# Kernel tuning notes

Hardware: AMD Instinct MI355X
Metric: run time of the kernel (lower is better)

The kernel has to match this reference:

```python
import jax, jax.numpy as jnp
import numpy as np

TOP_K = 32
OBS_RADIUS = 1.0
N = 4096
IN_DIM = 4


def setup_inputs() -> dict:
    key = jax.random.key(0)
    ks = jax.random.split(key, 10)
    s = 0.05
    return {
        "states": jax.random.normal(ks[0], (N, 4), jnp.float32),
        "goals": jax.random.normal(ks[1], (N, 2), jnp.float32),
        "W1": jax.random.normal(ks[2], (64, IN_DIM + 1), jnp.float32) * s,
        "b1": jnp.zeros((64,), jnp.float32),
        "W2": jax.random.normal(ks[3], (128, 64), jnp.float32) * s,
        "b2": jnp.zeros((128,), jnp.float32),
        "Wd1": jax.random.normal(ks[4], (64, 132), jnp.float32) * s,
        "bd1": jnp.zeros((64,), jnp.float32),
        "Wd2": jax.random.normal(ks[5], (128, 64), jnp.float32) * s,
        "bd2": jnp.zeros((128,), jnp.float32),
        "Wd3": jax.random.normal(ks[6], (64, 128), jnp.float32) * s,
        "bd3": jnp.zeros((64,), jnp.float32),
        "Wd4": jax.random.normal(ks[7], (4, 64), jnp.float32) * s,
        "bd4": jnp.zeros((4,), jnp.float32),
    }


def reference(states, goals, W1, b1, W2, b2, Wd1, bd1, Wd2, bd2, Wd3, bd3, Wd4, bd4):
    n = states.shape[0]
    dt = states.dtype
    # pairwise relative states + one-hot self indicator -> [N, N, 5]
    x = states[:, None, :] - states[None, :, :]
    x = jnp.concatenate([x, jnp.eye(n, dtype=dt)[:, :, None]], axis=2)
    # remove_distant_agents: keep TOP_K nearest neighbors by planar distance
    d = jnp.sqrt(jnp.sum(x[:, :, :2] ** 2, axis=2) + 1e-4)  # [N, N]
    _, idx = jax.lax.top_k(-d, TOP_K)                        # [N, K]
    xk = jnp.take_along_axis(x, idx[:, :, None], axis=1)     # [N, K, 5]
    # observation-radius mask (torch reshape [N,K,1]->[N,1,K] == transpose here)
    dist = jnp.linalg.norm(xk[:, :, :2], axis=2)             # [N, K]
    mask = (dist < OBS_RADIUS).astype(dt).reshape(n, 1, TOP_K)
    # NOTE: original uses a raw reshape [N,K,5]->[N,5,K] (not a transpose); match it
    h = xk.reshape(n, IN_DIM + 1, TOP_K)
    # pointwise (kernel-1) conv stack 5 -> 64 -> 128
    h = jax.nn.relu(jnp.einsum('oc,ncp->nop', W1, h) + b1[None, :, None])
    h = jax.nn.relu(jnp.einsum('oc,ncp->nop', W2, h) + b2[None, :, None])
    # original does torch.max(...)[1]: ARGMAX indices, promoted to float by cat
    x_local = jnp.argmax(h * mask, axis=2).astype(dt)        # [N, 128]
    rel = states[:, :2] - goals
    feat = jnp.concatenate([x_local, rel, states[:, 2:]], axis=1)  # [N, 132]
    z = jax.nn.relu(feat @ Wd1.T + bd1)
    z = jax.nn.relu(z @ Wd2.T + bd2)
    z = jax.nn.relu(z @ Wd3.T + bd3)
    z = z @ Wd4.T + bd4
    k = 2.0 * jax.nn.sigmoid(z) + 0.2                        # [N, 4] gains
    state = jnp.concatenate([rel, states[:, 2:]], axis=1)    # [N, 4]
    a_x = -(k[:, 0] * state[:, 0] + k[:, 1] * state[:, 2])
    a_y = -(k[:, 2] * state[:, 1] + k[:, 3] * state[:, 3])
    return jnp.stack([a_x, a_y], axis=1)                     # [N, 2]
```

## Files before the change

kernel.cpp:

```cpp
#include <hip/hip_runtime.h>
#include <math.h>

#define NAGENT 4096
#define TOPK 32
#define FAGB 8
#define CANDCAP 2048

__global__ __launch_bounds__(256) void topk_kernel(
    const float* __restrict__ states, int* __restrict__ idx_out)
{
    const int i = blockIdx.x;
    const int t = threadIdx.x;
    const int lane = t & 63;
    __shared__ unsigned int hist[1024];
    __shared__ unsigned int wsum[4];
    __shared__ unsigned long long cand[CANDCAP];
    __shared__ int ccount;
    __shared__ unsigned int cutB;

    #pragma unroll
    for (int u = 0; u < 4; ++u) hist[t + u * 256] = 0u;
    if (t == 0) ccount = 0;

    const float4 si = ((const float4*)states)[i];
    __syncthreads();

    unsigned int mybits[16];
    #pragma unroll
    for (int u = 0; u < 16; ++u) {
        int j = t + u * 256;
        float4 sj = ((const float4*)states)[j];
        float dx = __fsub_rn(si.x, sj.x);
        float dy = __fsub_rn(si.y, sj.y);
        float s  = __fadd_rn(__fadd_rn(__fmul_rn(dx, dx), __fmul_rn(dy, dy)), 1e-4f);
        float dv = sqrtf(s);
        mybits[u] = __float_as_uint(dv);
        unsigned int bin = (unsigned int)(dv * 256.0f);
        if (bin > 1023u) bin = 1023u;
        atomicAdd(&hist[bin], 1u);
    }
    __syncthreads();

    unsigned int h0 = hist[t * 4 + 0], h1 = hist[t * 4 + 1];
    unsigned int h2 = hist[t * 4 + 2], h3 = hist[t * 4 + 3];
    unsigned int v = h0 + h1 + h2 + h3;
    unsigned int inc = v;
    #pragma unroll
    for (int off = 1; off < 64; off <<= 1) {
        unsigned int u = __shfl_up(inc, off, 64);
        if (lane >= off) inc += u;
    }
    if (lane == 63) wsum[t >> 6] = inc;
    __syncthreads();
    unsigned int woff = 0;
    for (int w = 0; w < (t >> 6); ++w) woff += wsum[w];
    unsigned int incl = inc + woff;
    unsigned int exc  = incl - v;
    if (exc < TOPK && incl >= TOPK) {
        unsigned int cum = exc;
        unsigned int hh[4] = {h0, h1, h2, h3};
        int b = t * 4 + 3;
        #pragma unroll
        for (int q = 0; q < 4; ++q) {
            cum += hh[q];
            if (cum >= TOPK) { b = t * 4 + q; break; }
        }
        cutB = (unsigned int)b;
    }
    __syncthreads();

    const unsigned int B = cutB;
    #pragma unroll
    for (int u = 0; u < 16; ++u) {
        float dv = __uint_as_float(mybits[u]);
        unsigned int bin = (unsigned int)(dv * 256.0f);
        if (bin > 1023u) bin = 1023u;
        if (bin <= B) {
            int pos = atomicAdd(&ccount, 1);
            if (pos < CANDCAP)
                cand[pos] = ((unsigned long long)mybits[u] << 32)
                          | (unsigned int)(t + u * 256);
        }
    }
    __syncthreads();

    const int C = (ccount < CANDCAP) ? ccount : CANDCAP;
    for (int q = t; q < C; q += 256) {
        unsigned long long key = cand[q];
        int rank = 0;
        for (int r = 0; r < C; ++r) rank += (cand[r] < key) ? 1 : 0;
        if (rank < TOPK) idx_out[i * TOPK + rank] = (int)(key & 0xffffffffu);
    }
}

__global__ __launch_bounds__(256) void fused_kernel(
    const float* __restrict__ states, const float* __restrict__ goals,
    const float* __restrict__ W1,  const float* __restrict__ b1,
    const float* __restrict__ W2,  const float* __restrict__ b2,
    const float* __restrict__ Wd1, const float* __restrict__ bd1,
    const float* __restrict__ Wd2, const float* __restrict__ bd2,
    const float* __restrict__ Wd3, const float* __restrict__ bd3,
    const float* __restrict__ Wd4, const float* __restrict__ bd4,
    const int* __restrict__ idx_in, float* __restrict__ out)
{
    const int t = threadIdx.x;
    const int a = t >> 6;
    const int l = t & 63;
    const int base = blockIdx.x * FAGB;

    __shared__ __attribute__((aligned(16))) float w2a[64 * 68];
    __shared__ __attribute__((aligned(16))) float w2b[64 * 68];
    __shared__ __attribute__((aligned(16))) float w1s[320];
    __shared__ __attribute__((aligned(16))) float b1s[64];
    __shared__ __attribute__((aligned(16))) float b2s[128];
    __shared__ __attribute__((aligned(16))) float flat[4][160];
    __shared__ __attribute__((aligned(16))) float maskv[4][32];
    __shared__ __attribute__((aligned(16))) float featb[FAGB][132];
    __shared__ __attribute__((aligned(16))) float h1[4][2048];
    float* z1s = &h1[0][0];
    float* z2s = z1s + 512;
    float* z3s = z2s + 1024;
    float* kvs = z3s + 512;

    #pragma unroll
    for (int u = 0; u < 32; ++u) {
        int e = t + u * 256;
        int o = e >> 6, c = e & 63;
        float v = W2[e];
        int dst = c * 68 + ((o >> 3) << 2) + (o & 3);
        if (o & 4) w2b[dst] = v; else w2a[dst] = v;
    }
    for (int e = t; e < 320; e += 256) w1s[e] = W1[e];
    if (t < 64)  b1s[t] = b1[t];
    if (t < 128) b2s[t] = b2[t];
    __syncthreads();

    #pragma unroll
    for (int round = 0; round < 2; ++round) {
        const int g = round * 4 + a;
        const int i = base + g;

        if (l < 32) {
            int j = idx_in[i * TOPK + l];
            float4 sj  = ((const float4*)states)[j];
            float4 siv = ((const float4*)states)[i];
            float d0 = siv.x - sj.x;
            float d1 = siv.y - sj.y;
            float d2 = siv.z - sj.z;
            float d3 = siv.w - sj.w;
            flat[a][l * 5 + 0] = d0;
            flat[a][l * 5 + 1] = d1;
            flat[a][l * 5 + 2] = d2;
            flat[a][l * 5 + 3] = d3;
            flat[a][l * 5 + 4] = (j == i) ? 1.0f : 0.0f;
            float dist = sqrtf(__fadd_rn(__fmul_rn(d0, d0), __fmul_rn(d1, d1)));
            maskv[a][l] = (dist < 1.0f) ? 1.0f : 0.0f;
        } else if (l < 36) {
            int f = l - 32;
            float4 siv = ((const float4*)states)[i];
            float2 gi  = ((const float2*)goals)[i];
            float v = (f == 0) ? (siv.x - gi.x)
                    : (f == 1) ? (siv.y - gi.y)
                    : (f == 2) ? siv.z : siv.w;
            featb[g][128 + f] = v;
        }

        #pragma unroll
        for (int u = 0; u < 32; ++u) {
            int e = u * 64 + l;
            int p = e & 31, o1 = e >> 5;
            float acc = b1s[o1];
            #pragma unroll
            for (int f = 0; f < 5; ++f)
                acc += w1s[o1 * 5 + f] * flat[a][f * 32 + p];
            h1[a][o1 * 32 + p] = fmaxf(acc, 0.0f);
        }

        const int ow = l & 15;
        const int pt = l >> 4;
        float acc[8][8];
        #pragma unroll
        for (int k = 0; k < 8; ++k)
            #pragma unroll
            for (int q = 0; q < 8; ++q) acc[k][q] = 0.0f;

        for (int c4 = 0; c4 < 16; ++c4) {
            float4 wAv[4], wBv[4], hAv[4], hBv[4];
            #pragma unroll
            for (int cc = 0; cc < 4; ++cc) {
                int c = c4 * 4 + cc;
                wAv[cc] = *(const float4*)&w2a[c * 68 + ow * 4];
                wBv[cc] = *(const float4*)&w2b[c * 68 + ow * 4];
                hAv[cc] = *(const float4*)&h1[a][c * 32 + pt * 8];
                hBv[cc] = *(const float4*)&h1[a][c * 32 + pt * 8 + 4];
            }
            #pragma unroll
            for (int cc = 0; cc < 4; ++cc) {
                float wv[8] = {wAv[cc].x, wAv[cc].y, wAv[cc].z, wAv[cc].w,
                               wBv[cc].x, wBv[cc].y, wBv[cc].z, wBv[cc].w};
                float hv[8] = {hAv[cc].x, hAv[cc].y, hAv[cc].z, hAv[cc].w,
                               hBv[cc].x, hBv[cc].y, hBv[cc].z, hBv[cc].w};
                #pragma unroll
                for (int k = 0; k < 8; ++k)
                    #pragma unroll
                    for (int q = 0; q < 8; ++q)
                        acc[k][q] += wv[k] * hv[q];
            }
        }

        float4 mA = *(const float4*)&maskv[a][pt * 8];
        float4 mB = *(const float4*)&maskv[a][pt * 8 + 4];
        float mv[8] = {mA.x, mA.y, mA.z, mA.w, mB.x, mB.y, mB.z, mB.w};
        #pragma unroll
        for (int k = 0; k < 8; ++k) {
            float bb = b2s[ow * 8 + k];
            unsigned long long best = 0ull;
            #pragma unroll
            for (int q = 0; q < 8; ++q) {
                float val = fmaxf(acc[k][q] + bb, 0.0f) * mv[q];
                unsigned long long key =
                    ((unsigned long long)__float_as_uint(val) << 32)
                    | (unsigned int)(31 - (pt * 8 + q));
                if (key > best) best = key;
            }
            unsigned long long o1 = __shfl_xor(best, 16, 64); if (o1 > best) best = o1;
            unsigned long long o2 = __shfl_xor(best, 32, 64); if (o2 > best) best = o2;
            if (pt == 0) {
                int pbest = 31 - (int)(best & 63ull);
                featb[g][ow * 8 + k] = (float)pbest;
            }
        }
    }
    __syncthreads();

    const int g0 = 2 * a, g1 = 2 * a + 1;

    {
        float bb = bd1[l];
        float a0 = bb, a1 = bb;
        for (int k = 0; k < 33; ++k) {
            float4 wv = *(const float4*)&Wd1[l * 132 + 4 * k];
            float4 f0 = *(const float4*)&featb[g0][4 * k];
            float4 f1 = *(const float4*)&featb[g1][4 * k];
            a0 += wv.x * f0.x; a0 += wv.y * f0.y; a0 += wv.z * f0.z; a0 += wv.w * f0.w;
            a1 += wv.x * f1.x; a1 += wv.y * f1.y; a1 += wv.z * f1.z; a1 += wv.w * f1.w;
        }
        z1s[g0 * 64 + l] = fmaxf(a0, 0.0f);
        z1s[g1 * 64 + l] = fmaxf(a1, 0.0f);
    }

    {
        float accA0 = bd2[l], accA1 = bd2[l];
        float accB0 = bd2[l + 64], accB1 = bd2[l + 64];
        for (int k = 0; k < 16; ++k) {
            float4 wa = *(const float4*)&Wd2[l * 64 + 4 * k];
            float4 wb = *(const float4*)&Wd2[(l + 64) * 64 + 4 * k];
            float4 f0 = *(const float4*)&z1s[g0 * 64 + 4 * k];
            float4 f1 = *(const float4*)&z1s[g1 * 64 + 4 * k];
            accA0 += wa.x * f0.x; accA0 += wa.y * f0.y;
            accA0 += wa.z * f0.z; accA0 += wa.w * f0.w;
            accB0 += wb.x * f0.x; accB0 += wb.y * f0.y;
            accB0 += wb.z * f0.z; accB0 += wb.w * f0.w;
            accA1 += wa.x * f1.x; accA1 += wa.y * f1.y;
            accA1 += wa.z * f1.z; accA1 += wa.w * f1.w;
            accB1 += wb.x * f1.x; accB1 += wb.y * f1.y;
            accB1 += wb.z * f1.z; accB1 += wb.w * f1.w;
        }
        z2s[g0 * 128 + l]      = fmaxf(accA0, 0.0f);
        z2s[g0 * 128 + l + 64] = fmaxf(accB0, 0.0f);
        z2s[g1 * 128 + l]      = fmaxf(accA1, 0.0f);
        z2s[g1 * 128 + l + 64] = fmaxf(accB1, 0.0f);
    }

    {
        float bb = bd3[l];
        float a0 = bb, a1 = bb;
        for (int k = 0; k < 32; ++k) {
            float4 wv = *(const float4*)&Wd3[l * 128 + 4 * k];
            float4 f0 = *(const float4*)&z2s[g0 * 128 + 4 * k];
            float4 f1 = *(const float4*)&z2s[g1 * 128 + 4 * k];
            a0 += wv.x * f0.x; a0 += wv.y * f0.y; a0 += wv.z * f0.z; a0 += wv.w * f0.w;
            a1 += wv.x * f1.x; a1 += wv.y * f1.y; a1 += wv.z * f1.z; a1 += wv.w * f1.w;
        }
        z3s[g0 * 64 + l] = fmaxf(a0, 0.0f);
        z3s[g1 * 64 + l] = fmaxf(a1, 0.0f);
    }

    if (l < 8) {
        int gg = (l >> 2) ? g1 : g0;
        int o = l & 3;
        float acc = bd4[o];
        for (int c = 0; c < 64; ++c) acc += Wd4[o * 64 + c] * z3s[gg * 64 + c];
        kvs[gg * 4 + o] = 2.0f / (1.0f + expf(-acc)) + 0.2f;
    }
    if (l < 4) {
        int gg = (l >> 1) ? g1 : g0;
        int axis = l & 1;
        float ka = kvs[gg * 4 + 2 * axis + 0];
        float kb = kvs[gg * 4 + 2 * axis + 1];
        float rel = featb[gg][128 + axis];
        float vel = featb[gg][130 + axis];
        out[(base + gg) * 2 + axis] = -(ka * rel + kb * vel);
    }
}

extern "C" void kernel_launch(void* const* d_in, const int* in_sizes, int n_in,
                              void* d_out, int out_size, void* d_ws, size_t ws_size,
                              hipStream_t stream)
{
    const float* states = (const float*)d_in[0];
    const float* goals  = (const float*)d_in[1];
    const float* W1  = (const float*)d_in[2];
    const float* b1  = (const float*)d_in[3];
    const float* W2  = (const float*)d_in[4];
    const float* b2  = (const float*)d_in[5];
    const float* Wd1 = (const float*)d_in[6];
    const float* bd1 = (const float*)d_in[7];
    const float* Wd2 = (const float*)d_in[8];
    const float* bd2 = (const float*)d_in[9];
    const float* Wd3 = (const float*)d_in[10];
    const float* bd3 = (const float*)d_in[11];
    const float* Wd4 = (const float*)d_in[12];
    const float* bd4 = (const float*)d_in[13];

    int*   idx = (int*)d_ws;
    float* out = (float*)d_out;

    topk_kernel<<<NAGENT, 256, 0, stream>>>(states, idx);
    fused_kernel<<<NAGENT / FAGB, 256, 0, stream>>>(states, goals, W1, b1, W2, b2,
                                                    Wd1, bd1, Wd2, bd2, Wd3, bd3,
                                                    Wd4, bd4, idx, out);
}
```

Baseline: 141.0 us.

## Process all eight agents concurrently with 512-thread blocks and halved conv2 register tile

The fused kernel now launches 512 threads per block so each of eight wavefronts handles one agent, instead of four wavefronts looping over two rounds. The conv2 stage splits the 32 neighbor points into two 16-point halves, keeping a running argmax across halves, which halves the per-thread accumulator tile. The dense MLP tail then runs per-agent in each wavefront, with no block-wide sync before it. This removes serialization and register pressure in exchange for more shared memory per block and a launch-bounds occupancy request that may force spills.

```diff
diff --git a/kernel.cpp b/kernel.cpp
--- a/kernel.cpp
+++ b/kernel.cpp
@@ -93,7 +93,7 @@
     }
 }
 
-__global__ __launch_bounds__(256) void fused_kernel(
+__global__ __launch_bounds__(512, 4) void fused_kernel(
     const float* __restrict__ states, const float* __restrict__ goals,
     const float* __restrict__ W1,  const float* __restrict__ b1,
     const float* __restrict__ W2,  const float* __restrict__ b2,
@@ -107,200 +107,190 @@
     const int a = t >> 6;
     const int l = t & 63;
     const int base = blockIdx.x * FAGB;
+    const int i = base + a;
 
     __shared__ __attribute__((aligned(16))) float w2a[64 * 68];
     __shared__ __attribute__((aligned(16))) float w2b[64 * 68];
     __shared__ __attribute__((aligned(16))) float w1s[320];
     __shared__ __attribute__((aligned(16))) float b1s[64];
     __shared__ __attribute__((aligned(16))) float b2s[128];
-    __shared__ __attribute__((aligned(16))) float flat[4][160];
-    __shared__ __attribute__((aligned(16))) float maskv[4][32];
-    __shared__ __attribute__((aligned(16))) float featb[FAGB][132];
-    __shared__ __attribute__((aligned(16))) float h1[4][2048];
-    float* z1s = &h1[0][0];
-    float* z2s = z1s + 512;
-    float* z3s = z2s + 1024;
-    float* kvs = z3s + 512;
-
-    #pragma unroll
-    for (int u = 0; u < 32; ++u) {
-        int e = t + u * 256;
+    __shared__ __attribute__((aligned(16))) float flat[8][160];
+    __shared__ __attribute__((aligned(16))) float maskv[8][32];
+    __shared__ __attribute__((aligned(16))) float featb[8][132];
+    __shared__ __attribute__((aligned(16))) float h1p[8][1024];
+
+    if (l < 32) {
+        int j = idx_in[i * TOPK + l];
+        float4 sj  = ((const float4*)states)[j];
+        float4 siv = ((const float4*)states)[i];
+        float d0 = siv.x - sj.x;
+        float d1 = siv.y - sj.y;
+        float d2 = siv.z - sj.z;
+        float d3 = siv.w - sj.w;
+        flat[a][l * 5 + 0] = d0;
+        flat[a][l * 5 + 1] = d1;
+        flat[a][l * 5 + 2] = d2;
+        flat[a][l * 5 + 3] = d3;
+        flat[a][l * 5 + 4] = (j == i) ? 1.0f : 0.0f;
+        float dist = sqrtf(__fadd_rn(__fmul_rn(d0, d0), __fmul_rn(d1, d1)));
+        maskv[a][l] = (dist < 1.0f) ? 1.0f : 0.0f;
+    } else if (l < 36) {
+        int f = l - 32;
+        float4 siv = ((const float4*)states)[i];
+        float2 gi  = ((const float2*)goals)[i];
+        float v = (f == 0) ? (siv.x - gi.x)
+                : (f == 1) ? (siv.y - gi.y)
+                : (f == 2) ? siv.z : siv.w;
+        featb[a][128 + f] = v;
+    }
+
+    #pragma unroll
+    for (int u = 0; u < 16; ++u) {
+        int e = t + u * 512;
         int o = e >> 6, c = e & 63;
         float v = W2[e];
         int dst = c * 68 + ((o >> 3) << 2) + (o & 3);
         if (o & 4) w2b[dst] = v; else w2a[dst] = v;
     }
-    for (int e = t; e < 320; e += 256) w1s[e] = W1[e];
+    if (t < 320) w1s[t] = W1[t];
     if (t < 64)  b1s[t] = b1[t];
     if (t < 128) b2s[t] = b2[t];
     __syncthreads();
 
-    #pragma unroll
-    for (int round = 0; round < 2; ++round) {
-        const int g = round * 4 + a;
-        const int i = base + g;
-
-        if (l < 32) {
-            int j = idx_in[i * TOPK + l];
-            float4 sj  = ((const float4*)states)[j];
-            float4 siv = ((const float4*)states)[i];
-            float d0 = siv.x - sj.x;
-            float d1 = siv.y - sj.y;
-            float d2 = siv.z - sj.z;
-            float d3 = siv.w - sj.w;
-            flat[a][l * 5 + 0] = d0;
-            flat[a][l * 5 + 1] = d1;
-            flat[a][l * 5 + 2] = d2;
-            flat[a][l * 5 + 3] = d3;
-            flat[a][l * 5 + 4] = (j == i) ? 1.0f : 0.0f;
-            float dist = sqrtf(__fadd_rn(__fmul_rn(d0, d0), __fmul_rn(d1, d1)));
-            maskv[a][l] = (dist < 1.0f) ? 1.0f : 0.0f;
-        } else if (l < 36) {
-            int f = l - 32;
-            float4 siv = ((const float4*)states)[i];
-            float2 gi  = ((const float2*)goals)[i];
-            float v = (f == 0) ? (siv.x - gi.x)
-                    : (f == 1) ? (siv.y - gi.y)
-                    : (f == 2) ? siv.z : siv.w;
-            featb[g][128 + f] = v;
-        }
-
+    const int ow = l & 15;
+    const int ph = l >> 4;
+
+    float bb[8];
+    #pragma unroll
+    for (int k = 0; k < 8; ++k) bb[k] = b2s[ow * 8 + k];
+
+    unsigned long long rbest[8];
+    #pragma unroll
+    for (int k = 0; k < 8; ++k) rbest[k] = 0ull;
+
+    #pragma unroll
+    for (int pq = 0; pq < 2; ++pq) {
         #pragma unroll
-        for (int u = 0; u < 32; ++u) {
+        for (int u = 0; u < 16; ++u) {
             int e = u * 64 + l;
-            int p = e & 31, o1 = e >> 5;
+            int o1 = e >> 4, pp = e & 15;
             float acc = b1s[o1];
             #pragma unroll
             for (int f = 0; f < 5; ++f)
-                acc += w1s[o1 * 5 + f] * flat[a][f * 32 + p];
-            h1[a][o1 * 32 + p] = fmaxf(acc, 0.0f);
-        }
-
-        const int ow = l & 15;
-        const int pt = l >> 4;
-        float acc[8][8];
+                acc += w1s[o1 * 5 + f] * flat[a][f * 32 + pq * 16 + pp];
+            h1p[a][e] = fmaxf(acc, 0.0f);
+        }
+
+        float4 mv4 = *(const float4*)&maskv[a][pq * 16 + ph * 4];
+        float mv[4] = {mv4.x, mv4.y, mv4.z, mv4.w};
+
+        float acc[8][4];
         #pragma unroll
         for (int k = 0; k < 8; ++k)
             #pragma unroll
-            for (int q = 0; q < 8; ++q) acc[k][q] = 0.0f;
+            for (int q = 0; q < 4; ++q) acc[k][q] = 0.0f;
 
         for (int c4 = 0; c4 < 16; ++c4) {
-            float4 wAv[4], wBv[4], hAv[4], hBv[4];
+            float4 wAv[4], wBv[4], hv[4];
             #pragma unroll
             for (int cc = 0; cc < 4; ++cc) {
                 int c = c4 * 4 + cc;
                 wAv[cc] = *(const float4*)&w2a[c * 68 + ow * 4];
                 wBv[cc] = *(const float4*)&w2b[c * 68 + ow * 4];
-                hAv[cc] = *(const float4*)&h1[a][c * 32 + pt * 8];
-                hBv[cc] = *(const float4*)&h1[a][c * 32 + pt * 8 + 4];
+                hv[cc]  = *(const float4*)&h1p[a][c * 16 + ph * 4];
             }
             #pragma unroll
             for (int cc = 0; cc < 4; ++cc) {
                 float wv[8] = {wAv[cc].x, wAv[cc].y, wAv[cc].z, wAv[cc].w,
                                wBv[cc].x, wBv[cc].y, wBv[cc].z, wBv[cc].w};
-                float hv[8] = {hAv[cc].x, hAv[cc].y, hAv[cc].z, hAv[cc].w,
-                               hBv[cc].x, hBv[cc].y, hBv[cc].z, hBv[cc].w};
+                float hq[4] = {hv[cc].x, hv[cc].y, hv[cc].z, hv[cc].w};
                 #pragma unroll
                 for (int k = 0; k < 8; ++k)
                     #pragma unroll
-                    for (int q = 0; q < 8; ++q)
-                        acc[k][q] += wv[k] * hv[q];
+                    for (int q = 0; q < 4; ++q)
+                        acc[k][q] += wv[k] * hq[q];
             }
         }
 
-        float4 mA = *(const float4*)&maskv[a][pt * 8];
-        float4 mB = *(const float4*)&maskv[a][pt * 8 + 4];
-        float mv[8] = {mA.x, mA.y, mA.z, mA.w, mB.x, mB.y, mB.z, mB.w};
         #pragma unroll
         for (int k = 0; k < 8; ++k) {
-            float bb = b2s[ow * 8 + k];
-            unsigned long long best = 0ull;
-            #pragma unroll
-            for (int q = 0; q < 8; ++q) {
-                float val = fmaxf(acc[k][q] + bb, 0.0f) * mv[q];
+            unsigned long long best = rbest[k];
+            #pragma unroll
+            for (int q = 0; q < 4; ++q) {
+                float val = fmaxf(acc[k][q] + bb[k], 0.0f) * mv[q];
+                int p = pq * 16 + ph * 4 + q;
                 unsigned long long key =
                     ((unsigned long long)__float_as_uint(val) << 32)
-                    | (unsigned int)(31 - (pt * 8 + q));
+                    | (unsigned int)(31 - p);
                 if (key > best) best = key;
             }
-            unsigned long long o1 = __shfl_xor(best, 16, 64); if (o1 > best) best = o1;
-            unsigned long long o2 = __shfl_xor(best, 32, 64); if (o2 > best) best = o2;
-            if (pt == 0) {
-                int pbest = 31 - (int)(best & 63ull);
-                featb[g][ow * 8 + k] = (float)pbest;
-            }
-        }
-    }
-    __syncthreads();
-
-    const int g0 = 2 * a, g1 = 2 * a + 1;
+            rbest[k] = best;
+        }
+    }
+
+    #pragma unroll
+    for (int k = 0; k < 8; ++k) {
+        unsigned long long best = rbest[k];
+        unsigned long long o1 = __shfl_xor(best, 16, 64); if (o1 > best) best = o1;
+        unsigned long long o2 = __shfl_xor(best, 32, 64); if (o2 > best) best = o2;
+        if (ph == 0) {
+            int pbest = 31 - (int)(best & 63ull);
+            featb[a][ow * 8 + k] = (float)pbest;
+        }
+    }
+
+    float* z1s = &h1p[a][0];
+    float* z2s = z1s + 64;
+    float* z3s = z1s + 192;
+    float* kvs = z1s + 256;
 
     {
-        float bb = bd1[l];
-        float a0 = bb, a1 = bb;
+        float a0 = bd1[l];
         for (int k = 0; k < 33; ++k) {
             float4 wv = *(const float4*)&Wd1[l * 132 + 4 * k];
-            float4 f0 = *(const float4*)&featb[g0][4 * k];
-            float4 f1 = *(const float4*)&featb[g1][4 * k];
+            float4 f0 = *(const float4*)&featb[a][4 * k];
             a0 += wv.x * f0.x; a0 += wv.y * f0.y; a0 += wv.z * f0.z; a0 += wv.w * f0.w;
-            a1 += wv.x * f1.x; a1 += wv.y * f1.y; a1 += wv.z * f1.z; a1 += wv.w * f1.w;
-        }
-        z1s[g0 * 64 + l] = fmaxf(a0, 0.0f);
-        z1s[g1 * 64 + l] = fmaxf(a1, 0.0f);
+        }
+        z1s[l] = fmaxf(a0, 0.0f);
     }
 
     {
-        float accA0 = bd2[l], accA1 = bd2[l];
-        float accB0 = bd2[l + 64], accB1 = bd2[l + 64];
+        float accA = bd2[l];
+        float accB = bd2[l + 64];
         for (int k = 0; k < 16; ++k) {
             float4 wa = *(const float4*)&Wd2[l * 64 + 4 * k];
             float4 wb = *(const float4*)&Wd2[(l + 64) * 64 + 4 * k];
-            float4 f0 = *(const float4*)&z1s[g0 * 64 + 4 * k];
-            float4 f1 = *(const float4*)&z1s[g1 * 64 + 4 * k];
-            accA0 += wa.x * f0.x; accA0 += wa.y * f0.y;
-            accA0 += wa.z * f0.z; accA0 += wa.w * f0.w;
-            accB0 += wb.x * f0.x; accB0 += wb.y * f0.y;
-            accB0 += wb.z * f0.z; accB0 += wb.w * f0.w;
-            accA1 += wa.x * f1.x; accA1 += wa.y * f1.y;
-            accA1 += wa.z * f1.z; accA1 += wa.w * f1.w;
-            accB1 += wb.x * f1.x; accB1 += wb.y * f1.y;
-            accB1 += wb.z * f1.z; accB1 += wb.w * f1.w;
-        }
-        z2s[g0 * 128 + l]      = fmaxf(accA0, 0.0f);
-        z2s[g0 * 128 + l + 64] = fmaxf(accB0, 0.0f);
-        z2s[g1 * 128 + l]      = fmaxf(accA1, 0.0f);
-        z2s[g1 * 128 + l + 64] = fmaxf(accB1, 0.0f);
+            float4 f0 = *(const float4*)&z1s[4 * k];
+            accA += wa.x * f0.x; accA += wa.y * f0.y;
+            accA += wa.z * f0.z; accA += wa.w * f0.w;
+            accB += wb.x * f0.x; accB += wb.y * f0.y;
+            accB += wb.z * f0.z; accB += wb.w * f0.w;
+        }
+        z2s[l]      = fmaxf(accA, 0.0f);
+        z2s[l + 64] = fmaxf(accB, 0.0f);
     }
 
     {
-        float bb = bd3[l];
-        float a0 = bb, a1 = bb;
+        float a0 = bd3[l];
         for (int k = 0; k < 32; ++k) {
             float4 wv = *(const float4*)&Wd3[l * 128 + 4 * k];
-            float4 f0 = *(const float4*)&z2s[g0 * 128 + 4 * k];
-            float4 f1 = *(const float4*)&z2s[g1 * 128 + 4 * k];
+            float4 f0 = *(const float4*)&z2s[4 * k];
             a0 += wv.x * f0.x; a0 += wv.y * f0.y; a0 += wv.z * f0.z; a0 += wv.w * f0.w;
-            a1 += wv.x * f1.x; a1 += wv.y * f1.y; a1 += wv.z * f1.z; a1 += wv.w * f1.w;
-        }
-        z3s[g0 * 64 + l] = fmaxf(a0, 0.0f);
-        z3s[g1 * 64 + l] = fmaxf(a1, 0.0f);
-    }
-
-    if (l < 8) {
-        int gg = (l >> 2) ? g1 : g0;
-        int o = l & 3;
-        float acc = bd4[o];
-        for (int c = 0; c < 64; ++c) acc += Wd4[o * 64 + c] * z3s[gg * 64 + c];
-        kvs[gg * 4 + o] = 2.0f / (1.0f + expf(-acc)) + 0.2f;
-    }
+        }
+        z3s[l] = fmaxf(a0, 0.0f);
+    }
+
     if (l < 4) {
-        int gg = (l >> 1) ? g1 : g0;
-        int axis = l & 1;
-        float ka = kvs[gg * 4 + 2 * axis + 0];
-        float kb = kvs[gg * 4 + 2 * axis + 1];
-        float rel = featb[gg][128 + axis];
-        float vel = featb[gg][130 + axis];
-        out[(base + gg) * 2 + axis] = -(ka * rel + kb * vel);
+        float acc = bd4[l];
+        for (int c = 0; c < 64; ++c) acc += Wd4[l * 64 + c] * z3s[c];
+        kvs[l] = 2.0f / (1.0f + expf(-acc)) + 0.2f;
+    }
+    if (l < 2) {
+        float ka = kvs[2 * l + 0];
+        float kb = kvs[2 * l + 1];
+        float rel = featb[a][128 + l];
+        float vel = featb[a][130 + l];
+        out[i * 2 + l] = -(ka * rel + kb * vel);
     }
 }
 
@@ -327,7 +317,7 @@
     float* out = (float*)d_out;
 
     topk_kernel<<<NAGENT, 256, 0, stream>>>(states, idx);
-    fused_kernel<<<NAGENT / FAGB, 256, 0, stream>>>(states, goals, W1, b1, W2, b2,
+    fused_kernel<<<NAGENT / FAGB, 512, 0, stream>>>(states, goals, W1, b1, W2, b2,
                                                     Wd1, bd1, Wd2, bd2, Wd3, bd3,
                                                     Wd4, bd4, idx, out);
 }
```

Result: slower. 166.7 us (+18.2%).
